# Kernel tuning notes

Hardware: AMD Instinct MI355X
Metric: run time of the kernel (lower is better)

## Reference

```python
import jax, jax.numpy as jnp
import numpy as np

WH, WW = 8, 8
DIM, HEADS = 512, 16
HEAD_DIM = DIM // HEADS
SCALE = HEAD_DIM ** (-0.5)


def _rel_pos_index(wh, ww):
    # Swin relative position index, computed once with numpy (static).
    coords = np.stack(np.meshgrid(np.arange(wh), np.arange(ww), indexing='ij'))  # [2,wh,ww]
    cf = coords.reshape(2, -1)                                # [2, N]
    rel = cf[:, :, None] - cf[:, None, :]                     # [2, N, N]
    rel = rel.transpose(1, 2, 0).astype(np.int64)             # [N, N, 2]
    rel[..., 0] += wh - 1
    rel[..., 1] += ww - 1
    rel[..., 0] *= 2 * ww - 1
    return jnp.asarray(rel.sum(-1))                           # [N, N]

REL_IDX = _rel_pos_index(WH, WW)


def setup_inputs() -> dict:
    key = jax.random.key(0)
    ks = jax.random.split(key, 12)
    B_, N, C = 1024, WH * WW, DIM
    nW = 64
    std = C ** (-0.5)
    return {
        'q': jax.random.normal(ks[0], (B_, N, C), jnp.float32),
        'k': jax.random.normal(ks[1], (B_, N, C), jnp.float32),
        'v': jax.random.normal(ks[2], (B_, N, C), jnp.float32),
        'mask': jnp.zeros((nW, N, N), jnp.float32),
        'Wq': jax.random.normal(ks[3], (C, C), jnp.float32) * std,
        'bq': jnp.zeros((C,), jnp.float32),
        'Wk': jax.random.normal(ks[4], (C, C), jnp.float32) * std,
        'bk': jnp.zeros((C,), jnp.float32),
        'Wv': jax.random.normal(ks[5], (C, C), jnp.float32) * std,
        'bv': jnp.zeros((C,), jnp.float32),
        'Wp': jax.random.normal(ks[6], (C, C), jnp.float32) * std,
        'bp': jnp.zeros((C,), jnp.float32),
        'bias_table': jax.random.normal(ks[7], ((2 * WH - 1) * (2 * WW - 1), HEADS), jnp.float32) * 0.02,
    }


def reference(q, k, v, mask, Wq, bq, Wk, bk, Wv, bv, Wp, bp, bias_table):
    B_, N, C = q.shape
    H, hd = HEADS, HEAD_DIM

    def heads(x, W, b):  # Linear then split heads -> [B_, H, N, hd]
        return (x @ W.T + b).reshape(B_, N, H, hd).transpose(0, 2, 1, 3)

    qh = heads(q, Wq, bq) * SCALE
    kh = heads(k, Wk, bk)
    vh = heads(v, Wv, bv)

    attn = jnp.einsum('bhnd,bhmd->bhnm', qh, kh)              # [B_, H, N, N]
    rel_bias = bias_table[REL_IDX.reshape(-1)].reshape(N, N, H).transpose(2, 0, 1)  # [H,N,N]
    attn = attn + rel_bias[None]

    nW = mask.shape[0]
    attn = attn.reshape(B_ // nW, nW, H, N, N) + mask[None, :, None]
    attn = attn.reshape(B_, H, N, N)
    attn = jax.nn.softmax(attn, axis=-1)

    x = jnp.einsum('bhnm,bhmd->bhnd', attn, vh)
    x = x.transpose(0, 2, 1, 3).reshape(B_, N, C)
    return x @ Wp.T + bp
```

## Files before the change

kernel.cpp:

```cpp
#include <hip/hip_runtime.h>
#include <hip/hip_bf16.h>

typedef __attribute__((ext_vector_type(4))) float  f32x4;
typedef __attribute__((ext_vector_type(8))) short  bf16x8;
typedef __attribute__((ext_vector_type(4))) short  short4_t;
typedef unsigned short u16;

#define SCALE_Q 0.17677669529663687f

__device__ __forceinline__ short bfc(float f) {
    __bf16 b = (__bf16)f;
    union { __bf16 b; short s; } u; u.b = b; return u.s;
}

__device__ __forceinline__ void load_lds16(const void* g, void* l) {
    __builtin_amdgcn_global_load_lds(
        (const __attribute__((address_space(1))) void*)g,
        (__attribute__((address_space(3))) void*)l, 16, 0, 0);
}

__global__ __launch_bounds__(256) void cvt_kernel(
        const float* __restrict__ s, u16* __restrict__ d, int n8)
{
    const int i = blockIdx.x * 256 + threadIdx.x;
    if (i >= n8) return;
    const float4* sp = (const float4*)s + (size_t)i * 2;
    const float4 a = sp[0], b = sp[1];
    bf16x8 o;
    o[0] = bfc(a.x); o[1] = bfc(a.y); o[2] = bfc(a.z); o[3] = bfc(a.w);
    o[4] = bfc(b.x); o[5] = bfc(b.y); o[6] = bfc(b.z); o[7] = bfc(b.w);
    *((bf16x8*)d + i) = o;
}

__global__ __launch_bounds__(256) void wcvt_kernel(
        const float* __restrict__ w0, const float* __restrict__ w1,
        const float* __restrict__ w2, const float* __restrict__ w3,
        u16* __restrict__ d0, u16* __restrict__ d1,
        u16* __restrict__ d2, u16* __restrict__ d3)
{
    const float* s = (blockIdx.y == 0) ? w0 : (blockIdx.y == 1) ? w1
                   : (blockIdx.y == 2) ? w2 : w3;
    u16* d = (blockIdx.y == 0) ? d0 : (blockIdx.y == 1) ? d1
           : (blockIdx.y == 2) ? d2 : d3;
    const int i = blockIdx.x * 256 + threadIdx.x;
    const float4* sp = (const float4*)s + (size_t)i * 2;
    const float4 a = sp[0], b = sp[1];
    bf16x8 o;
    o[0] = bfc(a.x); o[1] = bfc(a.y); o[2] = bfc(a.z); o[3] = bfc(a.w);
    o[4] = bfc(b.x); o[5] = bfc(b.y); o[6] = bfc(b.z); o[7] = bfc(b.w);
    *((bf16x8*)d + i) = o;
}

__global__ __launch_bounds__(256) void cwb_kernel(
        const float* __restrict__ bias_table,
        const float* __restrict__ mask,
        float* __restrict__ cwb)
{
    const int wh = blockIdx.x;
    const int w = wh >> 4, h = wh & 15;
    for (int e = threadIdx.x; e < 4096; e += 256) {
        const int i = e >> 6, j = e & 63;
        const int rel = ((i >> 3) - (j >> 3) + 7) * 15 + (i & 7) - (j & 7) + 7;
        cwb[(size_t)wh * 4096 + e] = bias_table[rel * 16 + h] + mask[(size_t)w * 4096 + e];
    }
}

template<int OMODE>
__global__ __launch_bounds__(256) void gemm_b(
        const u16* __restrict__ A, const u16* __restrict__ Wb,
        const float* __restrict__ bias, float scale, void* __restrict__ outp)
{
    __shared__ __align__(16) u16 As[8192];
    __shared__ __align__(16) u16 Bs[8192];

    const int wg = (blockIdx.x & 7) * 256 + (blockIdx.x >> 3);
    const int m0 = (wg >> 2) << 7;
    const int n0 = (wg & 3) << 7;

    const int t = threadIdx.x;
    const int lane = t & 63, wv = t >> 6;
    const int g = lane >> 4, ln = lane & 15;
    const int wr = wv >> 1, wc = wv & 1;
    const int wbase = wv << 6;

    f32x4 acc[4][4];
#pragma unroll
    for (int i = 0; i < 4; i++)
#pragma unroll
        for (int j = 0; j < 4; j++) acc[i][j] = {0.f, 0.f, 0.f, 0.f};

    const u16* Abase = A  + (size_t)m0 * 512;
    const u16* Bbase = Wb + (size_t)n0 * 512;

    for (int k0 = 0; k0 < 512; k0 += 64) {
#pragma unroll
        for (int c = 0; c < 4; c++) {
            const int bi  = (c << 8) + wbase + lane;
            const int row = bi >> 3;
            const int cbs = (bi & 7) ^ (row & 7);
            const size_t go = (size_t)row * 512 + k0 + (cbs << 3);
            load_lds16(Abase + go, &As[((c << 8) + wbase) << 3]);
            load_lds16(Bbase + go, &Bs[((c << 8) + wbase) << 3]);
        }
        __syncthreads();
#pragma unroll
        for (int ks = 0; ks < 2; ks++) {
            bf16x8 af[4], bfr[4];
#pragma unroll
            for (int mt = 0; mt < 4; mt++) {
                const int row = (wr << 6) + (mt << 4) + ln;
                af[mt] = *(const bf16x8*)&As[(row << 6) + ((((ks << 2) + g) ^ (row & 7)) << 3)];
            }
#pragma unroll
            for (int nt = 0; nt < 4; nt++) {
                const int row = (wc << 6) + (nt << 4) + ln;
                bfr[nt] = *(const bf16x8*)&Bs[(row << 6) + ((((ks << 2) + g) ^ (row & 7)) << 3)];
            }
#pragma unroll
            for (int mt = 0; mt < 4; mt++)
#pragma unroll
                for (int nt = 0; nt < 4; nt++)
                    acc[mt][nt] = __builtin_amdgcn_mfma_f32_16x16x32_bf16(
                        af[mt], bfr[nt], acc[mt][nt], 0, 0, 0);
        }
        __syncthreads();
    }

#pragma unroll
    for (int mt = 0; mt < 4; mt++) {
#pragma unroll
        for (int nt = 0; nt < 4; nt++) {
            const int n = n0 + (wc << 6) + (nt << 4) + ln;
            const float bv = bias[n];
            const int mbase = m0 + (wr << 6) + (mt << 4) + (g << 2);
            if (OMODE == 0) {
#pragma unroll
                for (int r = 0; r < 4; r++) {
                    const int m = mbase + r;
                    const int b = m >> 6, tt = m & 63, hh = n >> 5, d = n & 31;
                    ((u16*)outp)[((size_t)(b * 16 + hh) * 64 + tt) * 32 + d] =
                        (u16)bfc((acc[mt][nt][r] + bv) * scale);
                }
            } else if (OMODE == 1) {
                short4_t hq;
#pragma unroll
                for (int r = 0; r < 4; r++) hq[r] = bfc((acc[mt][nt][r] + bv) * scale);
                const int b = mbase >> 6, tt = mbase & 63, hh = n >> 5, d = n & 31;
                *(short4_t*)&((u16*)outp)[((size_t)(b * 16 + hh) * 32 + d) * 64 + tt] = hq;
            } else {
#pragma unroll
                for (int r = 0; r < 4; r++) {
                    const int m = mbase + r;
                    ((float*)outp)[(size_t)m * 512 + n] = (acc[mt][nt][r] + bv) * scale;
                }
            }
        }
    }
}

__global__ __launch_bounds__(256) void attn_kernel(
        const u16* __restrict__ qh, const u16* __restrict__ kh,
        const u16* __restrict__ vt, const float* __restrict__ cwb,
        u16* __restrict__ xout)
{
    __shared__ __align__(16) u16 P[16384];

    const int wv = threadIdx.x >> 6;
    const int bid = (blockIdx.x << 2) + wv;
    const int b = bid >> 4, h = bid & 15, w = b & 63;
    const int lane = threadIdx.x & 63, g = lane >> 4, ln = lane & 15;
    const size_t base = (size_t)bid * 2048;
    u16* Pw = &P[wv << 12];

    bf16x8 vf[2][2];
#pragma unroll
    for (int ks = 0; ks < 2; ks++)
#pragma unroll
        for (int mt = 0; mt < 2; mt++)
            vf[ks][mt] = *(const bf16x8*)&vt[base + (mt * 16 + ln) * 64 + ks * 32 + g * 8];

    bf16x8 kf[4], qf[4];
#pragma unroll
    for (int mt = 0; mt < 4; mt++)
        kf[mt] = *(const bf16x8*)&kh[base + (mt * 16 + ln) * 32 + g * 8];
#pragma unroll
    for (int nt = 0; nt < 4; nt++)
        qf[nt] = *(const bf16x8*)&qh[base + (nt * 16 + ln) * 32 + g * 8];

    f32x4 acc[4][4];
#pragma unroll
    for (int i = 0; i < 4; i++)
#pragma unroll
        for (int j = 0; j < 4; j++) acc[i][j] = {0.f, 0.f, 0.f, 0.f};

#pragma unroll
    for (int mt = 0; mt < 4; mt++)
#pragma unroll
        for (int nt = 0; nt < 4; nt++)
            acc[mt][nt] = __builtin_amdgcn_mfma_f32_16x16x32_bf16(
                kf[mt], qf[nt], acc[mt][nt], 0, 0, 0);

    const float* cw = cwb + (size_t)(w * 16 + h) * 4096;
#pragma unroll
    for (int nt = 0; nt < 4; nt++) {
        const int i = nt * 16 + ln;
#pragma unroll
        for (int mt = 0; mt < 4; mt++) {
            const float4 bm = *(const float4*)&cw[i * 64 + mt * 16 + (g << 2)];
            acc[mt][nt][0] += bm.x; acc[mt][nt][1] += bm.y;
            acc[mt][nt][2] += bm.z; acc[mt][nt][3] += bm.w;
        }
    }

#pragma unroll
    for (int nt = 0; nt < 4; nt++) {
        float mx = acc[0][nt][0];
#pragma unroll
        for (int mt = 0; mt < 4; mt++)
#pragma unroll
            for (int r = 0; r < 4; r++) mx = fmaxf(mx, acc[mt][nt][r]);
        mx = fmaxf(mx, __shfl_xor(mx, 16));
        mx = fmaxf(mx, __shfl_xor(mx, 32));
        float sum = 0.f;
#pragma unroll
        for (int mt = 0; mt < 4; mt++)
#pragma unroll
            for (int r = 0; r < 4; r++) {
                const float p = __expf(acc[mt][nt][r] - mx);
                acc[mt][nt][r] = p;
                sum += p;
            }
        sum += __shfl_xor(sum, 16);
        sum += __shfl_xor(sum, 32);
        const float rs = 1.0f / sum;
        const int i = nt * 16 + ln;
#pragma unroll
        for (int mt = 0; mt < 4; mt++) {
            short4_t hq;
#pragma unroll
            for (int r = 0; r < 4; r++) hq[r] = bfc(acc[mt][nt][r] * rs);
            const int idx = (i * 64 + mt * 16 + (g << 2)) ^ ((i & 7) << 3);
            *(short4_t*)&Pw[idx] = hq;
        }
    }

    f32x4 oacc[2][4];
#pragma unroll
    for (int i = 0; i < 2; i++)
#pragma unroll
        for (int j = 0; j < 4; j++) oacc[i][j] = {0.f, 0.f, 0.f, 0.f};

#pragma unroll
    for (int ks = 0; ks < 2; ks++) {
        bf16x8 pf[4];
#pragma unroll
        for (int nt = 0; nt < 4; nt++) {
            const int i = nt * 16 + ln;
            pf[nt] = *(const bf16x8*)&Pw[(i * 64 + ks * 32 + g * 8) ^ ((i & 7) << 3)];
        }
#pragma unroll
        for (int mt = 0; mt < 2; mt++)
#pragma unroll
            for (int nt = 0; nt < 4; nt++)
                oacc[mt][nt] = __builtin_amdgcn_mfma_f32_16x16x32_bf16(
                    vf[ks][mt], pf[nt], oacc[mt][nt], 0, 0, 0);
    }

#pragma unroll
    for (int mt = 0; mt < 2; mt++) {
#pragma unroll
        for (int nt = 0; nt < 4; nt++) {
            const int i = nt * 16 + ln, d0 = mt * 16 + (g << 2);
            short4_t hq;
#pragma unroll
            for (int r = 0; r < 4; r++) hq[r] = bfc(oacc[mt][nt][r]);
            *(short4_t*)&xout[((size_t)b * 64 + i) * 512 + h * 32 + d0] = hq;
        }
    }
}

extern "C" void kernel_launch(void* const* d_in, const int* in_sizes, int n_in,
                              void* d_out, int out_size, void* d_ws, size_t ws_size,
                              hipStream_t stream) {
    const float* q    = (const float*)d_in[0];
    const float* k    = (const float*)d_in[1];
    const float* v    = (const float*)d_in[2];
    const float* mask = (const float*)d_in[3];
    const float* Wq   = (const float*)d_in[4];
    const float* bq   = (const float*)d_in[5];
    const float* Wk   = (const float*)d_in[6];
    const float* bk   = (const float*)d_in[7];
    const float* Wv   = (const float*)d_in[8];
    const float* bv   = (const float*)d_in[9];
    const float* Wp   = (const float*)d_in[10];
    const float* bp   = (const float*)d_in[11];
    const float* bias_table = (const float*)d_in[12];
    float* out = (float*)d_out;

    char* ws = (char*)d_ws;
    u16*   t0  = (u16*)(ws);
    u16*   qh  = (u16*)(ws + 67108864);
    u16*   kh  = (u16*)(ws + 134217728);
    u16*   vt  = (u16*)(ws + 201326592);
    float* cwb = (float*)(ws + 268435456);
    u16*   wqb = (u16*)(ws + 285212672);
    u16*   wkb = (u16*)(ws + 285736960);
    u16*   wvb = (u16*)(ws + 286261248);
    u16*   wpb = (u16*)(ws + 286785536);

    const int n8_act = (1024 * 64 * 512) / 8;

    cwb_kernel<<<1024, 256, 0, stream>>>(bias_table, mask, cwb);
    wcvt_kernel<<<dim3(128, 4), 256, 0, stream>>>(Wq, Wk, Wv, Wp, wqb, wkb, wvb, wpb);

    cvt_kernel<<<n8_act / 256, 256, 0, stream>>>(q, t0, n8_act);
    gemm_b<0><<<2048, 256, 0, stream>>>(t0, wqb, bq, SCALE_Q, (void*)qh);

    cvt_kernel<<<n8_act / 256, 256, 0, stream>>>(k, t0, n8_act);
    gemm_b<0><<<2048, 256, 0, stream>>>(t0, wkb, bk, 1.0f, (void*)kh);

    cvt_kernel<<<n8_act / 256, 256, 0, stream>>>(v, t0, n8_act);
    gemm_b<1><<<2048, 256, 0, stream>>>(t0, wvb, bv, 1.0f, (void*)vt);

    attn_kernel<<<4096, 256, 0, stream>>>(qh, kh, vt, cwb, t0);

    gemm_b<2><<<2048, 256, 0, stream>>>(t0, wpb, bp, 1.0f, (void*)out);
}
```

Baseline: 424.5 us.

## Double-buffer GEMM K tiles with async LDS prefetch and widen attention blocks

The projection GEMM now splits K into 32-wide tiles held in two LDS buffers. It prefetches the next tile with global_load_lds and waits on partial vmcnt, so global loads overlap the MFMA work, and it uses a new XOR swizzle for the narrower rows. Separately, the attention kernel moves from 4 to 8 waves per block, doubling its LDS allocation and halving the grid. The cost is more barrier iterations per GEMM and a larger LDS footprint per attention block, which may cut occupancy.

```diff
diff --git a/kernel.cpp b/kernel.cpp
--- a/kernel.cpp
+++ b/kernel.cpp
@@ -66,22 +66,24 @@
 }
 
 template<int OMODE>
-__global__ __launch_bounds__(256) void gemm_b(
+__global__ __launch_bounds__(256) void gemm_d(
         const u16* __restrict__ A, const u16* __restrict__ Wb,
         const float* __restrict__ bias, float scale, void* __restrict__ outp)
 {
-    __shared__ __align__(16) u16 As[8192];
-    __shared__ __align__(16) u16 Bs[8192];
+    __shared__ __align__(16) u16 As[2][4096];
+    __shared__ __align__(16) u16 Bs[2][4096];
 
     const int wg = (blockIdx.x & 7) * 256 + (blockIdx.x >> 3);
     const int m0 = (wg >> 2) << 7;
     const int n0 = (wg & 3) << 7;
 
     const int t = threadIdx.x;
-    const int lane = t & 63, wv = t >> 6;
+    const int lane = t & 63, wv_ = t >> 6;
     const int g = lane >> 4, ln = lane & 15;
-    const int wr = wv >> 1, wc = wv & 1;
-    const int wbase = wv << 6;
+    const int wr = wv_ >> 1, wc = wv_ & 1;
+
+    const u16* Ab = A  + (size_t)m0 * 512;
+    const u16* Bb = Wb + (size_t)n0 * 512;
 
     f32x4 acc[4][4];
 #pragma unroll
@@ -89,42 +91,55 @@
 #pragma unroll
         for (int j = 0; j < 4; j++) acc[i][j] = {0.f, 0.f, 0.f, 0.f};
 
-    const u16* Abase = A  + (size_t)m0 * 512;
-    const u16* Bbase = Wb + (size_t)n0 * 512;
-
-    for (int k0 = 0; k0 < 512; k0 += 64) {
-#pragma unroll
-        for (int c = 0; c < 4; c++) {
-            const int bi  = (c << 8) + wbase + lane;
-            const int row = bi >> 3;
-            const int cbs = (bi & 7) ^ (row & 7);
-            const size_t go = (size_t)row * 512 + k0 + (cbs << 3);
-            load_lds16(Abase + go, &As[((c << 8) + wbase) << 3]);
-            load_lds16(Bbase + go, &Bs[((c << 8) + wbase) << 3]);
-        }
-        __syncthreads();
-#pragma unroll
-        for (int ks = 0; ks < 2; ks++) {
-            bf16x8 af[4], bfr[4];
-#pragma unroll
-            for (int mt = 0; mt < 4; mt++) {
-                const int row = (wr << 6) + (mt << 4) + ln;
-                af[mt] = *(const bf16x8*)&As[(row << 6) + ((((ks << 2) + g) ^ (row & 7)) << 3)];
-            }
-#pragma unroll
-            for (int nt = 0; nt < 4; nt++) {
-                const int row = (wc << 6) + (nt << 4) + ln;
-                bfr[nt] = *(const bf16x8*)&Bs[(row << 6) + ((((ks << 2) + g) ^ (row & 7)) << 3)];
-            }
-#pragma unroll
-            for (int mt = 0; mt < 4; mt++)
-#pragma unroll
-                for (int nt = 0; nt < 4; nt++)
-                    acc[mt][nt] = __builtin_amdgcn_mfma_f32_16x16x32_bf16(
-                        af[mt], bfr[nt], acc[mt][nt], 0, 0, 0);
-        }
-        __syncthreads();
-    }
+#define STAGED(KT, BUF) do {                                                 \
+    _Pragma("unroll")                                                        \
+    for (int c = 0; c < 2; c++) {                                            \
+        const int bi = (c << 8) + t, row = bi >> 2, blk = bi & 3;            \
+        const int col = ((KT) << 5) + ((blk ^ ((row >> 1) & 3)) << 3);       \
+        load_lds16(Ab + (size_t)row * 512 + col, &As[BUF][bi << 3]);         \
+        load_lds16(Bb + (size_t)row * 512 + col, &Bs[BUF][bi << 3]);         \
+    }                                                                        \
+} while (0)
+
+#define COMPD(BUF) do {                                                      \
+    bf16x8 af[4], bfr[4];                                                    \
+    _Pragma("unroll")                                                        \
+    for (int mt = 0; mt < 4; mt++) {                                         \
+        const int rm = (wr << 6) + (mt << 4) + ln;                           \
+        const int sl = g ^ ((rm >> 1) & 3);                                  \
+        af[mt] = *(const bf16x8*)&As[BUF][(rm << 5) + (sl << 3)];            \
+    }                                                                        \
+    _Pragma("unroll")                                                        \
+    for (int nt = 0; nt < 4; nt++) {                                         \
+        const int rn = (wc << 6) + (nt << 4) + ln;                           \
+        const int sl = g ^ ((rn >> 1) & 3);                                  \
+        bfr[nt] = *(const bf16x8*)&Bs[BUF][(rn << 5) + (sl << 3)];           \
+    }                                                                        \
+    _Pragma("unroll")                                                        \
+    for (int mt = 0; mt < 4; mt++)                                           \
+        _Pragma("unroll")                                                    \
+        for (int nt = 0; nt < 4; nt++)                                       \
+            acc[mt][nt] = __builtin_amdgcn_mfma_f32_16x16x32_bf16(           \
+                af[mt], bfr[nt], acc[mt][nt], 0, 0, 0);                      \
+} while (0)
+
+    STAGED(0, 0);
+    for (int kt = 0; kt < 16; ++kt) {
+        if (kt < 15) {
+            if ((kt & 1) == 0) STAGED(kt + 1, 1); else STAGED(kt + 1, 0);
+            asm volatile("s_waitcnt vmcnt(4)" ::: "memory");
+        } else {
+            asm volatile("s_waitcnt vmcnt(0)" ::: "memory");
+        }
+        __builtin_amdgcn_s_barrier();
+        asm volatile("" ::: "memory");
+        if ((kt & 1) == 0) COMPD(0); else COMPD(1);
+        asm volatile("" ::: "memory");
+        __builtin_amdgcn_s_barrier();
+        asm volatile("" ::: "memory");
+    }
+#undef STAGED
+#undef COMPD
 
 #pragma unroll
     for (int mt = 0; mt < 4; mt++) {
@@ -158,15 +173,15 @@
     }
 }
 
-__global__ __launch_bounds__(256) void attn_kernel(
+__global__ __launch_bounds__(512) void attn_kernel(
         const u16* __restrict__ qh, const u16* __restrict__ kh,
         const u16* __restrict__ vt, const float* __restrict__ cwb,
         u16* __restrict__ xout)
 {
-    __shared__ __align__(16) u16 P[16384];
+    __shared__ __align__(16) u16 P[32768];
 
     const int wv = threadIdx.x >> 6;
-    const int bid = (blockIdx.x << 2) + wv;
+    const int bid = (blockIdx.x << 3) + wv;
     const int b = bid >> 4, h = bid & 15, w = b & 63;
     const int lane = threadIdx.x & 63, g = lane >> 4, ln = lane & 15;
     const size_t base = (size_t)bid * 2048;
@@ -314,15 +329,15 @@
     wcvt_kernel<<<dim3(128, 4), 256, 0, stream>>>(Wq, Wk, Wv, Wp, wqb, wkb, wvb, wpb);
 
     cvt_kernel<<<n8_act / 256, 256, 0, stream>>>(q, t0, n8_act);
-    gemm_b<0><<<2048, 256, 0, stream>>>(t0, wqb, bq, SCALE_Q, (void*)qh);
+    gemm_d<0><<<2048, 256, 0, stream>>>(t0, wqb, bq, SCALE_Q, (void*)qh);
 
     cvt_kernel<<<n8_act / 256, 256, 0, stream>>>(k, t0, n8_act);
-    gemm_b<0><<<2048, 256, 0, stream>>>(t0, wkb, bk, 1.0f, (void*)kh);
+    gemm_d<0><<<2048, 256, 0, stream>>>(t0, wkb, bk, 1.0f, (void*)kh);
 
     cvt_kernel<<<n8_act / 256, 256, 0, stream>>>(v, t0, n8_act);
-    gemm_b<1><<<2048, 256, 0, stream>>>(t0, wvb, bv, 1.0f, (void*)vt);
-
-    attn_kernel<<<4096, 256, 0, stream>>>(qh, kh, vt, cwb, t0);
-
-    gemm_b<2><<<2048, 256, 0, stream>>>(t0, wpb, bp, 1.0f, (void*)out);
-}
+    gemm_d<1><<<2048, 256, 0, stream>>>(t0, wvb, bv, 1.0f, (void*)vt);
+
+    attn_kernel<<<2048, 512, 0, stream>>>(qh, kh, vt, cwb, t0);
+
+    gemm_d<2><<<2048, 256, 0, stream>>>(t0, wpb, bp, 1.0f, (void*)out);
+}
```

Result: slower. 455.3 us (+7.2%).
